# Kernel tuning notes

Measured on AMD Instinct MI355X. Metric: run time of the kernel, lower is better.

The kernel has to match this reference:

```python
import jax, jax.numpy as jnp
import numpy as np

B, S, E, H = 4, 2048, 1024, 16
D = E // H  # head dim = 64


def setup_inputs() -> dict:
    key = jax.random.key(0)
    ks = jax.random.split(key, 9)
    s_in = 1.0 / np.sqrt(E)
    return {
        "x": jax.random.normal(ks[0], (B, S, E), dtype=jnp.float32),
        # stacked per-head projection weights, acting as x @ W + b
        "Wq": jax.random.normal(ks[1], (H, E, D), dtype=jnp.float32) * s_in,
        "bq": jax.random.normal(ks[2], (H, D), dtype=jnp.float32) * 0.01,
        "Wk": jax.random.normal(ks[3], (H, E, D), dtype=jnp.float32) * s_in,
        "bk": jax.random.normal(ks[4], (H, D), dtype=jnp.float32) * 0.01,
        "Wv": jax.random.normal(ks[5], (H, E, D), dtype=jnp.float32) * s_in,
        "bv": jax.random.normal(ks[6], (H, D), dtype=jnp.float32) * 0.01,
        "Wo": jax.random.normal(ks[7], (E, E), dtype=jnp.float32) * s_in,
        "bo": jax.random.normal(ks[8], (E,), dtype=jnp.float32) * 0.01,
    }


def reference(x, Wq, bq, Wk, bk, Wv, bv, Wo, bo):
    # Batched per-head projections (equivalent to the per-head nn.Linear loop)
    q = jnp.einsum("bse,hed->bhsd", x, Wq) + bq[None, :, None, :]
    k = jnp.einsum("bse,hed->bhsd", x, Wk) + bk[None, :, None, :]
    v = jnp.einsum("bse,hed->bhsd", x, Wv) + bv[None, :, None, :]
    scale = 1.0 / jnp.sqrt(jnp.asarray(D, dtype=x.dtype))
    scores = jnp.einsum("bhsd,bhtd->bhst", q, k) * scale  # [B,H,S,S]
    attn = jax.nn.softmax(scores, axis=-1)
    ctx = jnp.einsum("bhst,bhtd->bhsd", attn, v)  # [B,H,S,D]
    # torch.cat over heads along last dim -> [B,S,H*D]=[B,S,E]
    ctx = jnp.transpose(ctx, (0, 2, 1, 3)).reshape(x.shape[0], x.shape[1], E)
    return ctx @ Wo + bo
```

## Files before the change

### kernel.cpp

```cpp
#include <hip/hip_runtime.h>
#include <math.h>

#define B_ 4
#define S_ 2048
#define E_ 1024
#define H_ 16
#define D_ 64
#define BH_ (B_ * H_)

#define SCALE_LOG2E 0.18033688011112042f

typedef short short8 __attribute__((ext_vector_type(8)));
typedef float f32x4 __attribute__((ext_vector_type(4)));
typedef float f32x16 __attribute__((ext_vector_type(16)));

static __device__ __forceinline__ unsigned short f2bf(float f) {
    unsigned int u = __float_as_uint(f);
    unsigned int r = (u + 0x7fffu + ((u >> 16) & 1u)) >> 16;
    return (unsigned short)r;
}

static __device__ __forceinline__ unsigned int pack_bf16_trunc(float hi, float lo) {
    return __builtin_amdgcn_perm(__float_as_uint(hi), __float_as_uint(lo), 0x07060302u);
}

static __device__ __forceinline__ void gl_lds16(const unsigned short* g, unsigned short* l) {
    __builtin_amdgcn_global_load_lds(
        (const __attribute__((address_space(1))) unsigned int*)g,
        (__attribute__((address_space(3))) unsigned int*)l, 16, 0, 0);
}


__global__ __launch_bounds__(256) void xcvt_kernel(
    const float* __restrict__ x, unsigned short* __restrict__ Xb)
{
    size_t i = ((size_t)blockIdx.x * 256 + threadIdx.x) * 8;
    float4 a = *(const float4*)&x[i];
    float4 b = *(const float4*)&x[i + 4];
    ushort4 u0, u1;
    u0.x = f2bf(a.x); u0.y = f2bf(a.y); u0.z = f2bf(a.z); u0.w = f2bf(a.w);
    u1.x = f2bf(b.x); u1.y = f2bf(b.y); u1.z = f2bf(b.z); u1.w = f2bf(b.w);
    *(ushort4*)&Xb[i]     = u0;
    *(ushort4*)&Xb[i + 4] = u1;
}

__global__ __launch_bounds__(256) void wtrans_qkv_kernel(
    const float* __restrict__ Wq, const float* __restrict__ Wk,
    const float* __restrict__ Wv, unsigned short* __restrict__ Wt)
{
    __shared__ float t[32][33];
    const int tx = threadIdx.x & 31, ty = threadIdx.x >> 5;
    const int r0 = blockIdx.x * 32, c0 = blockIdx.y * 32;
    const int z = blockIdx.z, mtx = z >> 4, h = z & 15;
    const float* s = (mtx == 0 ? Wq : (mtx == 1 ? Wk : Wv)) + (size_t)h * E_ * D_;
    const float scale = (mtx == 0) ? SCALE_LOG2E : 1.0f;
    unsigned short* d = Wt + (size_t)mtx * E_ * E_ + (size_t)h * D_ * E_;
#pragma unroll
    for (int i = 0; i < 4; ++i)
        t[ty + i * 8][tx] = s[(size_t)(r0 + ty + i * 8) * D_ + c0 + tx];
    __syncthreads();
#pragma unroll
    for (int i = 0; i < 4; ++i)
        d[(size_t)(c0 + ty + i * 8) * E_ + r0 + tx] = f2bf(t[tx][ty + i * 8] * scale);
}

__global__ __launch_bounds__(256) void wtrans_kernel(
    const float* __restrict__ src, unsigned short* __restrict__ dst, int R, int C)
{
    __shared__ float t[32][33];
    const int tx = threadIdx.x & 31, ty = threadIdx.x >> 5;
    const int r0 = blockIdx.x * 32, c0 = blockIdx.y * 32;
#pragma unroll
    for (int i = 0; i < 4; ++i)
        t[ty + i * 8][tx] = src[(size_t)(r0 + ty + i * 8) * C + c0 + tx];
    __syncthreads();
#pragma unroll
    for (int i = 0; i < 4; ++i)
        dst[(size_t)(c0 + ty + i * 8) * R + r0 + tx] = f2bf(t[tx][ty + i * 8]);
}

__global__ __launch_bounds__(256) void qkv_gemm_kernel(
    const unsigned short* __restrict__ Xb, const unsigned short* __restrict__ Wt,
    const float* __restrict__ bq, const float* __restrict__ bk,
    const float* __restrict__ bv,
    unsigned short* __restrict__ Qh, unsigned short* __restrict__ Kh,
    unsigned short* __restrict__ Vth)
{
    __shared__ unsigned short As[2][128 * 64];
    __shared__ unsigned short Bs[2][128 * 64];
    const int tid = threadIdx.x;
    const int lane = tid & 63, wid = tid >> 6;
    const int quad = lane >> 4, lc = lane & 15;
    const int wm = wid >> 1, wn = wid & 1;
    const int m0 = blockIdx.y * 128, n0 = blockIdx.x * 128;
    const int l8 = lane >> 3;
    const int sch = ((lane & 7) ^ l8) * 8;

    f32x4 acc[4][4];
#pragma unroll
    for (int mt = 0; mt < 4; ++mt)
#pragma unroll
        for (int nt = 0; nt < 4; ++nt)
            acc[mt][nt] = (f32x4){0.f, 0.f, 0.f, 0.f};

#pragma unroll
    for (int i = 0; i < 4; ++i) {
        int rw = wid * 32 + i * 8;
        gl_lds16(&Xb[(size_t)(m0 + rw + l8) * E_ + sch], &As[0][rw * 64]);
        gl_lds16(&Wt[(size_t)(n0 + rw + l8) * E_ + sch], &Bs[0][rw * 64]);
    }
    __syncthreads();

    for (int k0 = 0; k0 < E_; k0 += 64) {
        const int cur = (k0 >> 6) & 1;
        if (k0 + 64 < E_) {
#pragma unroll
            for (int i = 0; i < 4; ++i) {
                int rw = wid * 32 + i * 8;
                gl_lds16(&Xb[(size_t)(m0 + rw + l8) * E_ + k0 + 64 + sch], &As[cur ^ 1][rw * 64]);
                gl_lds16(&Wt[(size_t)(n0 + rw + l8) * E_ + k0 + 64 + sch], &Bs[cur ^ 1][rw * 64]);
            }
        }
#pragma unroll
        for (int kc = 0; kc < 2; ++kc) {
            short8 a[4], bfr[4];
#pragma unroll
            for (int mt = 0; mt < 4; ++mt)
                a[mt] = *(const short8*)&As[cur][(wm * 64 + mt * 16 + lc) * 64 +
                                                (((kc * 4 + quad) ^ (lc & 7)) << 3)];
#pragma unroll
            for (int nt = 0; nt < 4; ++nt)
                bfr[nt] = *(const short8*)&Bs[cur][(wn * 64 + nt * 16 + lc) * 64 +
                                                  (((kc * 4 + quad) ^ (lc & 7)) << 3)];
#pragma unroll
            for (int mt = 0; mt < 4; ++mt)
#pragma unroll
                for (int nt = 0; nt < 4; ++nt)
                    acc[mt][nt] = __builtin_amdgcn_mfma_f32_16x16x32_bf16(
                        a[mt], bfr[nt], acc[mt][nt], 0, 0, 0);
        }
        __syncthreads();
    }

    const int nb = n0 + wn * 64;
    const int mtx = nb >> 10;
    const int h = (nb >> 6) & 15;
    const int sg0 = m0 + wm * 64;
    const int bb_ = sg0 >> 11;
    const int bhv = bb_ * H_ + h;
    if (mtx < 2) {
        const float bsc = (mtx == 0) ? SCALE_LOG2E : 1.0f;
        const float* bias = (mtx == 0 ? bq : bk) + h * D_;
        unsigned short* Out = (mtx == 0) ? Qh : Kh;
        const size_t obase = (size_t)bhv * (S_ / 32) * 2048;
#pragma unroll
        for (int nt = 0; nt < 4; ++nt) {
            int d = nt * 16 + lc;
            int hi_ = (lc >> 3) & 1, j = lc & 7;
            float bb = bias[d] * bsc;
#pragma unroll
            for (int mt = 0; mt < 4; ++mt)
#pragma unroll
                for (int r = 0; r < 4; ++r) {
                    int ss = (sg0 + mt * 16 + quad * 4 + r) & (S_ - 1);
                    Out[obase + ((size_t)(ss >> 5) * 4 + nt) * 512 +
                        ((ss & 31) * 2 + hi_) * 8 + j] = f2bf(acc[mt][nt][r] + bb);
                }
        }
    } else {
        const float* bias = bv + h * D_;
        const size_t obase = (size_t)bhv * (S_ / 64) * 4096;
        const int t64 = (sg0 & (S_ - 1)) >> 6;
        const int hi_ = quad >> 1, j0 = (quad & 1) * 4;
#pragma unroll
        for (int nt = 0; nt < 4; ++nt) {
            int d = nt * 16 + lc;
            int dsub = d >> 5, l31d = d & 31;
            float bb = bias[d];
#pragma unroll
            for (int mt = 0; mt < 4; ++mt) {
                ushort4 u;
                u.x = f2bf(acc[mt][nt][0] + bb);
                u.y = f2bf(acc[mt][nt][1] + bb);
                u.z = f2bf(acc[mt][nt][2] + bb);
                u.w = f2bf(acc[mt][nt][3] + bb);
                *(ushort4*)&Vth[obase + ((size_t)t64 * 8 + mt * 2 + dsub) * 512 +
                                (l31d * 2 + hi_) * 8 + j0] = u;
            }
        }
    }
}

__global__ __launch_bounds__(256, 4) void attn_kernel(
    const unsigned short* __restrict__ Qh, const unsigned short* __restrict__ Kh,
    const unsigned short* __restrict__ Vth, unsigned short* __restrict__ Ch)
{
    __shared__ unsigned short ks[2][8 * 512];
    __shared__ unsigned short vt[2][8 * 512];
    const int tid = threadIdx.x;
    const int lane = tid & 63, wid = tid >> 6;
    const int l31 = lane & 31, hi = lane >> 5;
    const int bh = blockIdx.x, b = bh >> 4, h = bh & 15;
    const int q0 = blockIdx.y * 128;
    const size_t gbase = (size_t)bh * (S_ / 32) * 2048;
    const int rdoff = (l31 * 2 + hi) * 8;
    const int ldoff = lane * 8;

    short8 qf[4];
    {
        const int t32 = (q0 >> 5) + wid;
#pragma unroll
        for (int kc = 0; kc < 4; ++kc)
            qf[kc] = *(const short8*)&Qh[gbase + ((size_t)t32 * 4 + kc) * 512 + rdoff];
    }

#pragma unroll
    for (int i = 0; i < 2; ++i) {
        int sk = wid * 2 + i;
        gl_lds16(&Kh[gbase + (size_t)sk * 512 + ldoff], &ks[0][sk * 512]);
        gl_lds16(&Vth[gbase + (size_t)sk * 512 + ldoff], &vt[0][sk * 512]);
    }
    __syncthreads();

    f32x16 ctx[2];
    float lsum = 0.f;
#pragma unroll
    for (int i = 0; i < 16; ++i) { ctx[0][i] = 0.f; ctx[1][i] = 0.f; }

    for (int kt = 0; kt < S_; kt += 64) {
        const int cur = (kt >> 6) & 1;
        if (kt + 64 < S_) {
            const int ktn = kt + 64;
#pragma unroll
            for (int i = 0; i < 2; ++i) {
                int sk = wid * 2 + i;
                gl_lds16(&Kh[gbase + ((size_t)((ktn >> 5) + (sk >> 2)) * 4 + (sk & 3)) * 512 + ldoff],
                         &ks[cur ^ 1][sk * 512]);
                gl_lds16(&Vth[gbase + ((size_t)(ktn >> 6) * 8 + sk) * 512 + ldoff],
                         &vt[cur ^ 1][sk * 512]);
            }
        }

        f32x16 st0, st1;
#pragma unroll
        for (int i = 0; i < 16; ++i) { st0[i] = 0.f; st1[i] = 0.f; }
        __builtin_amdgcn_s_setprio(1);
#pragma unroll
        for (int kc = 0; kc < 4; ++kc) {
            short8 kf0 = *(const short8*)&ks[cur][(0 * 4 + kc) * 512 + rdoff];
            st0 = __builtin_amdgcn_mfma_f32_32x32x16_bf16(kf0, qf[kc], st0, 0, 0, 0);
        }
#pragma unroll
        for (int kc = 0; kc < 4; ++kc) {
            short8 kf1 = *(const short8*)&ks[cur][(1 * 4 + kc) * 512 + rdoff];
            st1 = __builtin_amdgcn_mfma_f32_32x32x16_bf16(kf1, qf[kc], st1, 0, 0, 0);
        }
        __builtin_amdgcn_s_setprio(0);

        auto process = [&](const f32x16& ST, int KB) {
#pragma unroll
            for (int ks16 = 0; ks16 < 2; ++ks16) {
                float e0 = __builtin_amdgcn_exp2f(ST[8 * ks16 + 0]);
                float e1 = __builtin_amdgcn_exp2f(ST[8 * ks16 + 1]);
                float e2 = __builtin_amdgcn_exp2f(ST[8 * ks16 + 2]);
                float e3 = __builtin_amdgcn_exp2f(ST[8 * ks16 + 3]);
                float e4 = __builtin_amdgcn_exp2f(ST[8 * ks16 + 4]);
                float e5 = __builtin_amdgcn_exp2f(ST[8 * ks16 + 5]);
                float e6 = __builtin_amdgcn_exp2f(ST[8 * ks16 + 6]);
                float e7 = __builtin_amdgcn_exp2f(ST[8 * ks16 + 7]);
                lsum += ((e0 + e1) + (e2 + e3)) + ((e4 + e5) + (e6 + e7));
                unsigned int w0 = pack_bf16_trunc(e1, e0);
                unsigned int w1 = pack_bf16_trunc(e3, e2);
                unsigned int w2 = pack_bf16_trunc(e5, e4);
                unsigned int w3 = pack_bf16_trunc(e7, e6);
                asm("v_permlane32_swap_b32 %0, %1" : "+v"(w0), "+v"(w2));
                asm("v_permlane32_swap_b32 %0, %1" : "+v"(w1), "+v"(w3));
                union { unsigned int u[4]; short8 s; } pu;
                pu.u[0] = w0; pu.u[1] = w1; pu.u[2] = w2; pu.u[3] = w3;
                const short8 pf = pu.s;

                __builtin_amdgcn_s_setprio(1);
#pragma unroll
                for (int dsub = 0; dsub < 2; ++dsub) {
                    short8 vf = *(const short8*)&vt[cur][((KB * 2 + ks16) * 2 + dsub) * 512 + rdoff];
                    ctx[dsub] = __builtin_amdgcn_mfma_f32_32x32x16_bf16(
                        pf, vf, ctx[dsub], 0, 0, 0);
                }
                __builtin_amdgcn_s_setprio(0);
            }
        };
        process(st0, 0);
        process(st1, 1);
        __syncthreads();
    }

    float* lsh = (float*)&ks[0][0];
    {
        float a = lsum, bx = lsum;
        asm("v_permlane32_swap_b32 %0, %1" : "+v"(a), "+v"(bx));
        float ltot = lsum + (hi ? a : bx);
        if (hi == 0) lsh[wid * 32 + l31] = ltot;
    }
    __syncthreads();
#pragma unroll
    for (int r = 0; r < 16; ++r) {
        int qr = (r & 3) + ((r >> 2) << 3) + hi * 4;
        float inv = 1.f / lsh[wid * 32 + qr];
        int q = q0 + wid * 32 + qr;
        size_t rowbase = ((size_t)b * S_ + q) * E_ + h * D_;
        Ch[rowbase + l31]      = f2bf(ctx[0][r] * inv);
        Ch[rowbase + 32 + l31] = f2bf(ctx[1][r] * inv);
    }
}

__global__ __launch_bounds__(256) void out_proj_kernel(
    const unsigned short* __restrict__ Ch, const unsigned short* __restrict__ Wot,
    const float* __restrict__ bo, float* __restrict__ out)
{
    __shared__ unsigned short As[2][128 * 64];
    __shared__ unsigned short Bs[2][128 * 64];
    const int tid = threadIdx.x;
    const int lane = tid & 63, wid = tid >> 6;
    const int quad = lane >> 4, lc = lane & 15;
    const int wm = wid >> 1, wn = wid & 1;
    const int m0 = blockIdx.y * 128, n0 = blockIdx.x * 128;
    const int l8 = lane >> 3;
    const int sch = ((lane & 7) ^ l8) * 8;

    f32x4 acc[4][4];
#pragma unroll
    for (int mt = 0; mt < 4; ++mt)
#pragma unroll
        for (int nt = 0; nt < 4; ++nt)
            acc[mt][nt] = (f32x4){0.f, 0.f, 0.f, 0.f};

#pragma unroll
    for (int i = 0; i < 4; ++i) {
        int rw = wid * 32 + i * 8;
        gl_lds16(&Ch[(size_t)(m0 + rw + l8) * E_ + sch], &As[0][rw * 64]);
        gl_lds16(&Wot[(size_t)(n0 + rw + l8) * E_ + sch], &Bs[0][rw * 64]);
    }
    __syncthreads();

    for (int k0 = 0; k0 < E_; k0 += 64) {
        const int cur = (k0 >> 6) & 1;
        if (k0 + 64 < E_) {
#pragma unroll
            for (int i = 0; i < 4; ++i) {
                int rw = wid * 32 + i * 8;
                gl_lds16(&Ch[(size_t)(m0 + rw + l8) * E_ + k0 + 64 + sch], &As[cur ^ 1][rw * 64]);
                gl_lds16(&Wot[(size_t)(n0 + rw + l8) * E_ + k0 + 64 + sch], &Bs[cur ^ 1][rw * 64]);
            }
        }
#pragma unroll
        for (int kc = 0; kc < 2; ++kc) {
            short8 a[4], bfr[4];
#pragma unroll
            for (int mt = 0; mt < 4; ++mt)
                a[mt] = *(const short8*)&As[cur][(wm * 64 + mt * 16 + lc) * 64 +
                                                (((kc * 4 + quad) ^ (lc & 7)) << 3)];
#pragma unroll
            for (int nt = 0; nt < 4; ++nt)
                bfr[nt] = *(const short8*)&Bs[cur][(wn * 64 + nt * 16 + lc) * 64 +
                                                  (((kc * 4 + quad) ^ (lc & 7)) << 3)];
#pragma unroll
            for (int mt = 0; mt < 4; ++mt)
#pragma unroll
                for (int nt = 0; nt < 4; ++nt)
                    acc[mt][nt] = __builtin_amdgcn_mfma_f32_16x16x32_bf16(
                        a[mt], bfr[nt], acc[mt][nt], 0, 0, 0);
        }
        __syncthreads();
    }

#pragma unroll
    for (int mt = 0; mt < 4; ++mt)
#pragma unroll
        for (int nt = 0; nt < 4; ++nt) {
            int n = n0 + wn * 64 + nt * 16 + lc;
            float bb = bo[n];
#pragma unroll
            for (int r = 0; r < 4; ++r) {
                int row = m0 + wm * 64 + mt * 16 + quad * 4 + r;
                out[(size_t)row * E_ + n] = acc[mt][nt][r] + bb;
            }
        }
}

extern "C" void kernel_launch(void* const* d_in, const int* in_sizes, int n_in,
                              void* d_out, int out_size, void* d_ws, size_t ws_size,
                              hipStream_t stream)
{
    const float* x  = (const float*)d_in[0];
    const float* Wq = (const float*)d_in[1];
    const float* bq = (const float*)d_in[2];
    const float* Wk = (const float*)d_in[3];
    const float* bk = (const float*)d_in[4];
    const float* Wv = (const float*)d_in[5];
    const float* bv = (const float*)d_in[6];
    const float* Wo = (const float*)d_in[7];
    const float* bo = (const float*)d_in[8];
    (void)in_sizes; (void)n_in; (void)out_size; (void)ws_size;

    const size_t N = (size_t)BH_ * S_ * D_;
    unsigned short* Wt  = (unsigned short*)d_ws;
    unsigned short* Wot = Wt + (size_t)3072 * 1024;
    unsigned short* Xb  = Wot + (size_t)1024 * 1024;
    unsigned short* Qh  = Xb + N;
    unsigned short* Kh  = Qh + N;
    unsigned short* Vth = Kh + N;
    unsigned short* Ch  = Vth + N;

    xcvt_kernel<<<dim3(4096), 256, 0, stream>>>(x, Xb);
    wtrans_qkv_kernel<<<dim3(32, 2, 48), 256, 0, stream>>>(Wq, Wk, Wv, Wt);
    wtrans_kernel<<<dim3(32, 32, 1), 256, 0, stream>>>(Wo, Wot, E_, E_);

    qkv_gemm_kernel<<<dim3(24, 64), 256, 0, stream>>>(Xb, Wt, bq, bk, bv, Qh, Kh, Vth);
    attn_kernel<<<dim3(64, 16), 256, 0, stream>>>(Qh, Kh, Vth, Ch);
    out_proj_kernel<<<dim3(8, 64), 256, 0, stream>>>(Ch, Wot, bo, (float*)d_out);
}
```

Measured before the change: 273.1 us.

## Software-pipeline attention QK^T ahead of softmax-PV with triple-buffered LDS

```diff
diff --git a/kernel.cpp b/kernel.cpp
--- a/kernel.cpp
+++ b/kernel.cpp
@@ -191,17 +191,17 @@
     }
 }
 
-__global__ __launch_bounds__(256, 4) void attn_kernel(
+__global__ __launch_bounds__(512, 4) void attn_kernel(
     const unsigned short* __restrict__ Qh, const unsigned short* __restrict__ Kh,
     const unsigned short* __restrict__ Vth, unsigned short* __restrict__ Ch)
 {
-    __shared__ unsigned short ks[2][8 * 512];
-    __shared__ unsigned short vt[2][8 * 512];
+    __shared__ unsigned short ks[3][8 * 512];
+    __shared__ unsigned short vt[3][8 * 512];
     const int tid = threadIdx.x;
     const int lane = tid & 63, wid = tid >> 6;
     const int l31 = lane & 31, hi = lane >> 5;
     const int bh = blockIdx.x, b = bh >> 4, h = bh & 15;
-    const int q0 = blockIdx.y * 128;
+    const int q0 = blockIdx.y * 256;
     const size_t gbase = (size_t)bh * (S_ / 32) * 2048;
     const int rdoff = (l31 * 2 + hi) * 8;
     const int ldoff = lane * 8;
@@ -215,10 +215,11 @@
     }
 
 #pragma unroll
-    for (int i = 0; i < 2; ++i) {
-        int sk = wid * 2 + i;
-        gl_lds16(&Kh[gbase + (size_t)sk * 512 + ldoff], &ks[0][sk * 512]);
-        gl_lds16(&Vth[gbase + (size_t)sk * 512 + ldoff], &vt[0][sk * 512]);
+    for (int tt = 0; tt < 2; ++tt) {
+        gl_lds16(&Kh[gbase + ((size_t)(tt * 2 + (wid >> 2)) * 4 + (wid & 3)) * 512 + ldoff],
+                 &ks[tt][wid * 512]);
+        gl_lds16(&Vth[gbase + ((size_t)tt * 8 + wid) * 512 + ldoff],
+                 &vt[tt][wid * 512]);
     }
     __syncthreads();
 
@@ -227,70 +228,82 @@
 #pragma unroll
     for (int i = 0; i < 16; ++i) { ctx[0][i] = 0.f; ctx[1][i] = 0.f; }
 
-    for (int kt = 0; kt < S_; kt += 64) {
-        const int cur = (kt >> 6) & 1;
-        if (kt + 64 < S_) {
-            const int ktn = kt + 64;
-#pragma unroll
-            for (int i = 0; i < 2; ++i) {
-                int sk = wid * 2 + i;
-                gl_lds16(&Kh[gbase + ((size_t)((ktn >> 5) + (sk >> 2)) * 4 + (sk & 3)) * 512 + ldoff],
-                         &ks[cur ^ 1][sk * 512]);
-                gl_lds16(&Vth[gbase + ((size_t)(ktn >> 6) * 8 + sk) * 512 + ldoff],
-                         &vt[cur ^ 1][sk * 512]);
-            }
-        }
-
-        f32x16 st0, st1;
-#pragma unroll
-        for (int i = 0; i < 16; ++i) { st0[i] = 0.f; st1[i] = 0.f; }
+    f32x16 stH;
+#pragma unroll
+    for (int i = 0; i < 16; ++i) stH[i] = 0.f;
+#pragma unroll
+    for (int kc = 0; kc < 4; ++kc) {
+        short8 kf = *(const short8*)&ks[0][kc * 512 + rdoff];
+        stH = __builtin_amdgcn_mfma_f32_32x32x16_bf16(kf, qf[kc], stH, 0, 0, 0);
+    }
+
+    auto smpv = [&](const f32x16& ST, int buf, int KB) {
+#pragma unroll
+        for (int ks16 = 0; ks16 < 2; ++ks16) {
+            float e0 = __builtin_amdgcn_exp2f(ST[8 * ks16 + 0]);
+            float e1 = __builtin_amdgcn_exp2f(ST[8 * ks16 + 1]);
+            float e2 = __builtin_amdgcn_exp2f(ST[8 * ks16 + 2]);
+            float e3 = __builtin_amdgcn_exp2f(ST[8 * ks16 + 3]);
+            float e4 = __builtin_amdgcn_exp2f(ST[8 * ks16 + 4]);
+            float e5 = __builtin_amdgcn_exp2f(ST[8 * ks16 + 5]);
+            float e6 = __builtin_amdgcn_exp2f(ST[8 * ks16 + 6]);
+            float e7 = __builtin_amdgcn_exp2f(ST[8 * ks16 + 7]);
+            lsum += ((e0 + e1) + (e2 + e3)) + ((e4 + e5) + (e6 + e7));
+            unsigned int w0 = pack_bf16_trunc(e1, e0);
+            unsigned int w1 = pack_bf16_trunc(e3, e2);
+            unsigned int w2 = pack_bf16_trunc(e5, e4);
+            unsigned int w3 = pack_bf16_trunc(e7, e6);
+            asm("v_permlane32_swap_b32 %0, %1" : "+v"(w0), "+v"(w2));
+            asm("v_permlane32_swap_b32 %0, %1" : "+v"(w1), "+v"(w3));
+            union { unsigned int u[4]; short8 s; } pu;
+            pu.u[0] = w0; pu.u[1] = w1; pu.u[2] = w2; pu.u[3] = w3;
+            const short8 pf = pu.s;
+#pragma unroll
+            for (int dsub = 0; dsub < 2; ++dsub) {
+                short8 vf = *(const short8*)&vt[buf][((KB * 2 + ks16) * 2 + dsub) * 512 + rdoff];
+                ctx[dsub] = __builtin_amdgcn_mfma_f32_32x32x16_bf16(
+                    pf, vf, ctx[dsub], 0, 0, 0);
+            }
+        }
+    };
+
+    const int NT = S_ / 64;
+    for (int t = 0; t < NT; ++t) {
+        const int cur = t % 3, nxt = (t + 1) % 3, stg = (t + 2) % 3;
+        if (t + 2 < NT) {
+            gl_lds16(&Kh[gbase + ((size_t)((t + 2) * 2 + (wid >> 2)) * 4 + (wid & 3)) * 512 + ldoff],
+                     &ks[stg][wid * 512]);
+            gl_lds16(&Vth[gbase + ((size_t)(t + 2) * 8 + wid) * 512 + ldoff],
+                     &vt[stg][wid * 512]);
+        }
+
+        f32x16 stN;
+#pragma unroll
+        for (int i = 0; i < 16; ++i) stN[i] = 0.f;
         __builtin_amdgcn_s_setprio(1);
 #pragma unroll
         for (int kc = 0; kc < 4; ++kc) {
-            short8 kf0 = *(const short8*)&ks[cur][(0 * 4 + kc) * 512 + rdoff];
-            st0 = __builtin_amdgcn_mfma_f32_32x32x16_bf16(kf0, qf[kc], st0, 0, 0, 0);
-        }
-#pragma unroll
-        for (int kc = 0; kc < 4; ++kc) {
-            short8 kf1 = *(const short8*)&ks[cur][(1 * 4 + kc) * 512 + rdoff];
-            st1 = __builtin_amdgcn_mfma_f32_32x32x16_bf16(kf1, qf[kc], st1, 0, 0, 0);
+            short8 kf = *(const short8*)&ks[cur][(4 + kc) * 512 + rdoff];
+            stN = __builtin_amdgcn_mfma_f32_32x32x16_bf16(kf, qf[kc], stN, 0, 0, 0);
         }
         __builtin_amdgcn_s_setprio(0);
-
-        auto process = [&](const f32x16& ST, int KB) {
-#pragma unroll
-            for (int ks16 = 0; ks16 < 2; ++ks16) {
-                float e0 = __builtin_amdgcn_exp2f(ST[8 * ks16 + 0]);
-                float e1 = __builtin_amdgcn_exp2f(ST[8 * ks16 + 1]);
-                float e2 = __builtin_amdgcn_exp2f(ST[8 * ks16 + 2]);
-                float e3 = __builtin_amdgcn_exp2f(ST[8 * ks16 + 3]);
-                float e4 = __builtin_amdgcn_exp2f(ST[8 * ks16 + 4]);
-                float e5 = __builtin_amdgcn_exp2f(ST[8 * ks16 + 5]);
-                float e6 = __builtin_amdgcn_exp2f(ST[8 * ks16 + 6]);
-                float e7 = __builtin_amdgcn_exp2f(ST[8 * ks16 + 7]);
-                lsum += ((e0 + e1) + (e2 + e3)) + ((e4 + e5) + (e6 + e7));
-                unsigned int w0 = pack_bf16_trunc(e1, e0);
-                unsigned int w1 = pack_bf16_trunc(e3, e2);
-                unsigned int w2 = pack_bf16_trunc(e5, e4);
-                unsigned int w3 = pack_bf16_trunc(e7, e6);
-                asm("v_permlane32_swap_b32 %0, %1" : "+v"(w0), "+v"(w2));
-                asm("v_permlane32_swap_b32 %0, %1" : "+v"(w1), "+v"(w3));
-                union { unsigned int u[4]; short8 s; } pu;
-                pu.u[0] = w0; pu.u[1] = w1; pu.u[2] = w2; pu.u[3] = w3;
-                const short8 pf = pu.s;
-
-                __builtin_amdgcn_s_setprio(1);
-#pragma unroll
-                for (int dsub = 0; dsub < 2; ++dsub) {
-                    short8 vf = *(const short8*)&vt[cur][((KB * 2 + ks16) * 2 + dsub) * 512 + rdoff];
-                    ctx[dsub] = __builtin_amdgcn_mfma_f32_32x32x16_bf16(
-                        pf, vf, ctx[dsub], 0, 0, 0);
-                }
-                __builtin_amdgcn_s_setprio(0);
-            }
-        };
-        process(st0, 0);
-        process(st1, 1);
+        smpv(stH, cur, 0);
+        stH = stN;
+
+#pragma unroll
+        for (int i = 0; i < 16; ++i) stN[i] = 0.f;
+        if (t + 1 < NT) {
+            __builtin_amdgcn_s_setprio(1);
+#pragma unroll
+            for (int kc = 0; kc < 4; ++kc) {
+                short8 kf = *(const short8*)&ks[nxt][kc * 512 + rdoff];
+                stN = __builtin_amdgcn_mfma_f32_32x32x16_bf16(kf, qf[kc], stN, 0, 0, 0);
+            }
+            __builtin_amdgcn_s_setprio(0);
+        }
+        smpv(stH, cur, 1);
+        stH = stN;
+
         __syncthreads();
     }
 
@@ -416,6 +429,6 @@
     wtrans_kernel<<<dim3(32, 32, 1), 256, 0, stream>>>(Wo, Wot, E_, E_);
 
     qkv_gemm_kernel<<<dim3(24, 64), 256, 0, stream>>>(Xb, Wt, bq, bk, bv, Qh, Kh, Vth);
-    attn_kernel<<<dim3(64, 16), 256, 0, stream>>>(Qh, Kh, Vth, Ch);
+    attn_kernel<<<dim3(64, 8), 512, 0, stream>>>(Qh, Kh, Vth, Ch);
     out_proj_kernel<<<dim3(8, 64), 256, 0, stream>>>(Ch, Wot, bo, (float*)d_out);
 }
```

New measurement: 271.3 us. No clear change (-0.7%).
